# Kernel optimization log

Hardware: AMD Instinct MI355X
Metric: run time of the kernel (lower is better)

Reference implementation:

```python
import jax, jax.numpy as jnp
import numpy as np

N = 50000      # number of predictions
E = 1_600_000  # total neighborhood entries (sum of neighborhood sizes)
D = 128        # prediction representation dim
A = 4          # additional per-pair info dim (box offsets / IoU)
H = 128        # block hidden dim


def setup_inputs() -> dict:
    key = jax.random.key(0)
    ks = jax.random.split(key, 16)
    interpolated = jax.random.normal(ks[0], (N, D), dtype=jnp.float32)
    add_info = jax.random.normal(ks[1], (E, A), dtype=jnp.float32)
    neighbor_idx = jax.random.randint(ks[2], (E,), 0, N, dtype=jnp.int32)
    segment_ids = jnp.sort(jax.random.randint(ks[3], (E,), 0, N, dtype=jnp.int32))
    w = lambda k, shape: (jax.random.normal(k, shape, dtype=jnp.float32) * 0.02)
    return {
        "interpolated": interpolated,
        "add_info": add_info,
        "neighbor_idx": neighbor_idx,
        "segment_ids": segment_ids,
        "Wb0": w(ks[4], (D + A, H)), "bb0": jnp.zeros((H,), jnp.float32),
        "Wo0": w(ks[5], (H, D)),     "bo0": jnp.zeros((D,), jnp.float32),
        "Wb1": w(ks[6], (D + A, H)), "bb1": jnp.zeros((H,), jnp.float32),
        "Wo1": w(ks[7], (H, D)),     "bo1": jnp.zeros((D,), jnp.float32),
        "Wf": w(ks[8], (D, 1)),      "bf": jnp.zeros((1,), jnp.float32),
    }


def reference(interpolated, add_info, neighbor_idx, segment_ids,
              Wb0, bb0, Wo0, bo0, Wb1, bb1, Wo1, bo1, Wf, bf):
    def block_step(feats, Wb, bb, Wo, bo):
        # assemble all neighborhoods: gather neighbor reps, concat pair info -> (E, D+A)
        edge_feats = jnp.concatenate([feats[neighbor_idx], add_info], axis=-1)
        # block MLP on neighborhood entries -> (E, H)
        h = jax.nn.relu(edge_feats @ Wb + bb)
        # segment-wise max pool over each prediction's neighborhood -> (N, H)
        pooled = jax.ops.segment_max(h, segment_ids, num_segments=N)
        pooled = jnp.where(jnp.isfinite(pooled), pooled, 0.0)  # empty segments -> 0
        # output projection back to representation space, residual update
        return feats + (pooled @ Wo + bo)

    x = block_step(interpolated, Wb0, bb0, Wo0, bo0)
    x = block_step(x, Wb1, bb1, Wo1, bo1)
    # final layers: compress representation to updated objectness score -> (N, 1)
    return x @ Wf + bf
```

## Files before the change

### kernel.cpp

```cpp
#include <hip/hip_runtime.h>
#include <limits.h>
#include <cstdint>

typedef __bf16 bf16_t;
typedef __attribute__((ext_vector_type(8))) __bf16 bf16x8;
typedef __attribute__((ext_vector_type(4))) float f32x4;
typedef __attribute__((ext_vector_type(2))) float f32x2;

#define CH 64

struct PackArgs {
  const float* W[4];
  bf16_t* P[4];
};

__global__ __launch_bounds__(256) void pack4_kernel(PackArgs args) {
  int idx = blockIdx.x * blockDim.x + threadIdx.x;
  int which = idx >> 14;
  int r = idx & 16383;
  int j  = r & 7;
  int L  = (r >> 3) & 63;
  int nt = (r >> 9) & 7;
  int kt = r >> 12;
  int k = kt * 32 + (L >> 4) * 8 + j;
  int n = nt * 16 + (L & 15);
  args.P[which][r] = (bf16_t)args.W[which][(size_t)k * 128 + n];
}

__global__ __launch_bounds__(256, 4) void yproj_f32(
    const float* __restrict__ X, const bf16_t* __restrict__ Wtpk,
    bf16_t* __restrict__ Ybf, float* __restrict__ pooled, int N)
{
  const int tid = threadIdx.x;
  const int base = blockIdx.x * 128;

  float4 z = make_float4(0.f, 0.f, 0.f, 0.f);
  #pragma unroll
  for (int i = 0; i < 16; ++i) {
    int idx = tid + i * 256;
    int row = base + (idx >> 5);
    if (row < N)
      reinterpret_cast<float4*>(pooled)[(size_t)row * 32 + (idx & 31)] = z;
  }

  const int lane = tid & 63;
  const int w    = tid >> 6;
  const int q    = lane >> 4;
  const int ln   = lane & 15;
  const int n0   = base + w * 32;

  int r0 = n0 + ln, r1 = n0 + 16 + ln;
  int r0c = (r0 < N) ? r0 : (N - 1);
  int r1c = (r1 < N) ? r1 : (N - 1);
  const float* x0 = X + (size_t)r0c * 128 + q * 8;
  const float* x1 = X + (size_t)r1c * 128 + q * 8;

  f32x4 acc[2][8];
  #pragma unroll
  for (int mt = 0; mt < 2; ++mt)
    #pragma unroll
    for (int nt = 0; nt < 8; ++nt)
      #pragma unroll
      for (int r = 0; r < 4; ++r) acc[mt][nt][r] = 0.f;

  const bf16x8* Wp = reinterpret_cast<const bf16x8*>(Wtpk);
  #pragma unroll
  for (int kt = 0; kt < 4; ++kt) {
    float4 f0a = *reinterpret_cast<const float4*>(x0 + kt * 32);
    float4 f0b = *reinterpret_cast<const float4*>(x0 + kt * 32 + 4);
    float4 f1a = *reinterpret_cast<const float4*>(x1 + kt * 32);
    float4 f1b = *reinterpret_cast<const float4*>(x1 + kt * 32 + 4);
    bf16x8 a0, a1;
    a0[0] = (bf16_t)f0a.x; a0[1] = (bf16_t)f0a.y; a0[2] = (bf16_t)f0a.z; a0[3] = (bf16_t)f0a.w;
    a0[4] = (bf16_t)f0b.x; a0[5] = (bf16_t)f0b.y; a0[6] = (bf16_t)f0b.z; a0[7] = (bf16_t)f0b.w;
    a1[0] = (bf16_t)f1a.x; a1[1] = (bf16_t)f1a.y; a1[2] = (bf16_t)f1a.z; a1[3] = (bf16_t)f1a.w;
    a1[4] = (bf16_t)f1b.x; a1[5] = (bf16_t)f1b.y; a1[6] = (bf16_t)f1b.z; a1[7] = (bf16_t)f1b.w;
    #pragma unroll
    for (int nt = 0; nt < 8; ++nt) {
      bf16x8 bfrag = Wp[(kt * 8 + nt) * 64 + lane];
      acc[0][nt] = __builtin_amdgcn_mfma_f32_16x16x32_bf16(a0, bfrag, acc[0][nt], 0, 0, 0);
      acc[1][nt] = __builtin_amdgcn_mfma_f32_16x16x32_bf16(a1, bfrag, acc[1][nt], 0, 0, 0);
    }
  }

  #pragma unroll
  for (int mt = 0; mt < 2; ++mt) {
    #pragma unroll
    for (int r = 0; r < 4; ++r) {
      int row = n0 + mt * 16 + q * 4 + r;
      if (row < N) {
        #pragma unroll
        for (int nt = 0; nt < 8; ++nt) {
          int col = nt * 16 + ln;
          Ybf[(size_t)row * 128 + col] = (bf16_t)acc[mt][nt][r];
        }
      }
    }
  }
}

__global__ __launch_bounds__(256, 4) void yproj_bf16(
    const bf16_t* __restrict__ Xbf, const bf16_t* __restrict__ Wtpk,
    bf16_t* __restrict__ Ybf, float* __restrict__ pooled, int N)
{
  const int tid = threadIdx.x;
  const int base = blockIdx.x * 128;

  float4 z = make_float4(0.f, 0.f, 0.f, 0.f);
  #pragma unroll
  for (int i = 0; i < 16; ++i) {
    int idx = tid + i * 256;
    int row = base + (idx >> 5);
    if (row < N)
      reinterpret_cast<float4*>(pooled)[(size_t)row * 32 + (idx & 31)] = z;
  }

  const int lane = tid & 63;
  const int w    = tid >> 6;
  const int q    = lane >> 4;
  const int ln   = lane & 15;
  const int n0   = base + w * 32;

  int r0 = n0 + ln, r1 = n0 + 16 + ln;
  int r0c = (r0 < N) ? r0 : (N - 1);
  int r1c = (r1 < N) ? r1 : (N - 1);
  const bf16_t* x0 = Xbf + (size_t)r0c * 128 + q * 8;
  const bf16_t* x1 = Xbf + (size_t)r1c * 128 + q * 8;

  f32x4 acc[2][8];
  #pragma unroll
  for (int mt = 0; mt < 2; ++mt)
    #pragma unroll
    for (int nt = 0; nt < 8; ++nt)
      #pragma unroll
      for (int r = 0; r < 4; ++r) acc[mt][nt][r] = 0.f;

  const bf16x8* Wp = reinterpret_cast<const bf16x8*>(Wtpk);
  #pragma unroll
  for (int kt = 0; kt < 4; ++kt) {
    bf16x8 a0 = *reinterpret_cast<const bf16x8*>(x0 + kt * 32);
    bf16x8 a1 = *reinterpret_cast<const bf16x8*>(x1 + kt * 32);
    #pragma unroll
    for (int nt = 0; nt < 8; ++nt) {
      bf16x8 bfrag = Wp[(kt * 8 + nt) * 64 + lane];
      acc[0][nt] = __builtin_amdgcn_mfma_f32_16x16x32_bf16(a0, bfrag, acc[0][nt], 0, 0, 0);
      acc[1][nt] = __builtin_amdgcn_mfma_f32_16x16x32_bf16(a1, bfrag, acc[1][nt], 0, 0, 0);
    }
  }

  #pragma unroll
  for (int mt = 0; mt < 2; ++mt) {
    #pragma unroll
    for (int r = 0; r < 4; ++r) {
      int row = n0 + mt * 16 + q * 4 + r;
      if (row < N) {
        #pragma unroll
        for (int nt = 0; nt < 8; ++nt) {
          int col = nt * 16 + ln;
          Ybf[(size_t)row * 128 + col] = (bf16_t)acc[mt][nt][r];
        }
      }
    }
  }
}

__global__ __launch_bounds__(256) void edge_stream(
    const bf16_t* __restrict__ Y,
    const float* __restrict__ Wb,
    const float* __restrict__ bb,
    const float* __restrict__ add_info,
    const int* __restrict__ nbr, const int* __restrict__ segs,
    float* __restrict__ pooled, int E)
{
  __shared__ float a_lds[1024];
  const int lane = threadIdx.x & 63;
  const int wv = __builtin_amdgcn_readfirstlane(threadIdx.x >> 6);
  const int e0 = (blockIdx.x * 4 + wv) * CH;
  if (e0 >= E) return;
  const int c0 = lane * 2;

  f32x2 wk[4];
  #pragma unroll
  for (int k = 0; k < 4; ++k) {
    wk[k].x = Wb[(size_t)(128 + k) * 128 + c0];
    wk[k].y = Wb[(size_t)(128 + k) * 128 + c0 + 1];
  }
  f32x2 bbv;
  bbv.x = bb[c0]; bbv.y = bb[c0 + 1];

  unsigned* pooled_u = reinterpret_cast<unsigned*>(pooled);
  f32x2 v; v.x = 0.f; v.y = 0.f;

  if (e0 + CH <= E) {
    float4 av = *reinterpret_cast<const float4*>(add_info + (size_t)e0 * 4 + lane * 4);
    int v_nbr = nbr[e0 + lane];
    int v_sg  = segs[e0 + lane];

    int sg_prev = __shfl_up(v_sg, 1);
    unsigned long long bmask = __ballot(v_sg != sg_prev) & ~1ull;
    int cur = __builtin_amdgcn_readlane(v_sg, 0);

    unsigned ybuf[4][8];
    #pragma unroll
    for (int p = 0; p < 3; ++p) {
      #pragma unroll
      for (int j = 0; j < 8; ++j) {
        int rn = __builtin_amdgcn_readlane(v_nbr, p * 8 + j);
        ybuf[p][j] = *((const unsigned*)(Y + (size_t)rn * 128) + lane);
      }
    }

    *reinterpret_cast<float4*>(a_lds + wv * 256 + lane * 4) = av;

    #pragma unroll
    for (int g = 0; g < CH / 8; ++g) {
      if (g + 3 < CH / 8) {
        #pragma unroll
        for (int j = 0; j < 8; ++j) {
          int rn = __builtin_amdgcn_readlane(v_nbr, (g + 3) * 8 + j);
          ybuf[(g + 3) & 3][j] = *((const unsigned*)(Y + (size_t)rn * 128) + lane);
        }
      }
      #pragma unroll
      for (int j = 0; j < 8; ++j) {
        const int i = g * 8 + j;
        if (bmask & (1ull << i)) {
          if (v.x > 0.f) atomicMax(&pooled_u[(size_t)cur * 128 + c0], __float_as_uint(v.x));
          if (v.y > 0.f) atomicMax(&pooled_u[(size_t)cur * 128 + c0 + 1], __float_as_uint(v.y));
          v.x = 0.f; v.y = 0.f;
          cur = __builtin_amdgcn_readlane(v_sg, i);
        }
        unsigned yb = ybuf[g & 3][j];
        f32x2 y;
        y.x = __uint_as_float(yb << 16);
        y.y = __uint_as_float(yb & 0xffff0000u);
        f32x4 a4 = *reinterpret_cast<const f32x4*>(a_lds + wv * 256 + i * 4);
        f32x2 t = bbv + a4[0] * wk[0];
        t += a4[1] * wk[1];
        t += a4[2] * wk[2];
        t += a4[3] * wk[3];
        t += y;
        v = __builtin_elementwise_max(v, t);
      }
    }
    if (v.x > 0.f) atomicMax(&pooled_u[(size_t)cur * 128 + c0], __float_as_uint(v.x));
    if (v.y > 0.f) atomicMax(&pooled_u[(size_t)cur * 128 + c0 + 1], __float_as_uint(v.y));
  } else {
    int cur = segs[e0];
    const int rem = E - e0;
    for (int i = 0; i < rem; ++i) {
      const int e = e0 + i;
      int sg = segs[e];
      if (sg != cur) {
        if (v.x > 0.f) atomicMax(&pooled_u[(size_t)cur * 128 + c0], __float_as_uint(v.x));
        if (v.y > 0.f) atomicMax(&pooled_u[(size_t)cur * 128 + c0 + 1], __float_as_uint(v.y));
        v.x = 0.f; v.y = 0.f; cur = sg;
      }
      unsigned yb = *reinterpret_cast<const unsigned*>(Y + (size_t)nbr[e] * 128 + c0);
      float y0 = __uint_as_float(yb << 16);
      float y1 = __uint_as_float(yb & 0xffff0000u);
      const float* ai = add_info + (size_t)e * 4;
      float a0 = ai[0], a1 = ai[1], a2 = ai[2], a3 = ai[3];
      float t0 = y0 + bbv.x + a0 * wk[0].x + a1 * wk[1].x + a2 * wk[2].x + a3 * wk[3].x;
      float t1 = y1 + bbv.y + a0 * wk[0].y + a1 * wk[1].y + a2 * wk[2].y + a3 * wk[3].y;
      v.x = fmaxf(v.x, t0);
      v.y = fmaxf(v.y, t1);
    }
    if (v.x > 0.f) atomicMax(&pooled_u[(size_t)cur * 128 + c0], __float_as_uint(v.x));
    if (v.y > 0.f) atomicMax(&pooled_u[(size_t)cur * 128 + c0 + 1], __float_as_uint(v.y));
  }
}

__global__ __launch_bounds__(256, 4) void update_mfma(
    const float* __restrict__ featsIn, const float* __restrict__ pooled,
    const bf16_t* __restrict__ Wopk, const float* __restrict__ bo,
    const float* __restrict__ Wf,
    float* __restrict__ featsOut, bf16_t* __restrict__ featsOutBf,
    float* __restrict__ fdot, int N)
{
  const int tid  = threadIdx.x;
  const int lane = tid & 63;
  const int w    = tid >> 6;
  const int q    = lane >> 4;
  const int ln   = lane & 15;
  const int n0   = blockIdx.x * 128 + w * 32;

  int r0 = n0 + ln, r1 = n0 + 16 + ln;
  int r0c = (r0 < N) ? r0 : (N - 1);
  int r1c = (r1 < N) ? r1 : (N - 1);
  const float* p0 = pooled + (size_t)r0c * 128 + q * 8;
  const float* p1 = pooled + (size_t)r1c * 128 + q * 8;

  f32x4 acc[2][8];
  #pragma unroll
  for (int mt = 0; mt < 2; ++mt)
    #pragma unroll
    for (int nt = 0; nt < 8; ++nt)
      #pragma unroll
      for (int r = 0; r < 4; ++r) acc[mt][nt][r] = 0.f;

  const bf16x8* Wp = reinterpret_cast<const bf16x8*>(Wopk);
  #pragma unroll
  for (int kt = 0; kt < 4; ++kt) {
    float4 f0a = *reinterpret_cast<const float4*>(p0 + kt * 32);
    float4 f0b = *reinterpret_cast<const float4*>(p0 + kt * 32 + 4);
    float4 f1a = *reinterpret_cast<const float4*>(p1 + kt * 32);
    float4 f1b = *reinterpret_cast<const float4*>(p1 + kt * 32 + 4);
    bf16x8 a0, a1;
    a0[0] = (bf16_t)f0a.x; a0[1] = (bf16_t)f0a.y; a0[2] = (bf16_t)f0a.z; a0[3] = (bf16_t)f0a.w;
    a0[4] = (bf16_t)f0b.x; a0[5] = (bf16_t)f0b.y; a0[6] = (bf16_t)f0b.z; a0[7] = (bf16_t)f0b.w;
    a1[0] = (bf16_t)f1a.x; a1[1] = (bf16_t)f1a.y; a1[2] = (bf16_t)f1a.z; a1[3] = (bf16_t)f1a.w;
    a1[4] = (bf16_t)f1b.x; a1[5] = (bf16_t)f1b.y; a1[6] = (bf16_t)f1b.z; a1[7] = (bf16_t)f1b.w;
    #pragma unroll
    for (int nt = 0; nt < 8; ++nt) {
      bf16x8 bfrag = Wp[(kt * 8 + nt) * 64 + lane];
      acc[0][nt] = __builtin_amdgcn_mfma_f32_16x16x32_bf16(a0, bfrag, acc[0][nt], 0, 0, 0);
      acc[1][nt] = __builtin_amdgcn_mfma_f32_16x16x32_bf16(a1, bfrag, acc[1][nt], 0, 0, 0);
    }
  }

  float bov[8], wfv[8];
  #pragma unroll
  for (int nt = 0; nt < 8; ++nt) { bov[nt] = bo[nt * 16 + ln]; wfv[nt] = Wf[nt * 16 + ln]; }

  #pragma unroll
  for (int mt = 0; mt < 2; ++mt) {
    #pragma unroll
    for (int r = 0; r < 4; ++r) {
      int row = n0 + mt * 16 + q * 4 + r;
      float partial = 0.f;
      if (row < N) {
        #pragma unroll
        for (int nt = 0; nt < 8; ++nt) {
          int col = nt * 16 + ln;
          float o = featsIn[(size_t)row * 128 + col] + acc[mt][nt][r] + bov[nt];
          featsOut[(size_t)row * 128 + col] = o;
          featsOutBf[(size_t)row * 128 + col] = (bf16_t)o;
          partial += o * wfv[nt];
        }
      }
      partial += __shfl_xor(partial, 1);
      partial += __shfl_xor(partial, 2);
      partial += __shfl_xor(partial, 4);
      partial += __shfl_xor(partial, 8);
      if (ln == 0 && row < N) fdot[row] = partial;
    }
  }
}

__global__ __launch_bounds__(256, 4) void update_final_mfma(
    const float* __restrict__ fdot, const float* __restrict__ pooled,
    const bf16_t* __restrict__ Wopk, const float* __restrict__ bo,
    const float* __restrict__ Wf, const float* __restrict__ bf_,
    float* __restrict__ out, int N)
{
  const int tid  = threadIdx.x;
  const int lane = tid & 63;
  const int w    = tid >> 6;
  const int q    = lane >> 4;
  const int ln   = lane & 15;
  const int n0   = blockIdx.x * 128 + w * 32;

  int r0 = n0 + ln, r1 = n0 + 16 + ln;
  int r0c = (r0 < N) ? r0 : (N - 1);
  int r1c = (r1 < N) ? r1 : (N - 1);
  const float* p0 = pooled + (size_t)r0c * 128 + q * 8;
  const float* p1 = pooled + (size_t)r1c * 128 + q * 8;

  f32x4 acc[2][8];
  #pragma unroll
  for (int mt = 0; mt < 2; ++mt)
    #pragma unroll
    for (int nt = 0; nt < 8; ++nt)
      #pragma unroll
      for (int r = 0; r < 4; ++r) acc[mt][nt][r] = 0.f;

  const bf16x8* Wp = reinterpret_cast<const bf16x8*>(Wopk);
  #pragma unroll
  for (int kt = 0; kt < 4; ++kt) {
    float4 f0a = *reinterpret_cast<const float4*>(p0 + kt * 32);
    float4 f0b = *reinterpret_cast<const float4*>(p0 + kt * 32 + 4);
    float4 f1a = *reinterpret_cast<const float4*>(p1 + kt * 32);
    float4 f1b = *reinterpret_cast<const float4*>(p1 + kt * 32 + 4);
    bf16x8 a0, a1;
    a0[0] = (bf16_t)f0a.x; a0[1] = (bf16_t)f0a.y; a0[2] = (bf16_t)f0a.z; a0[3] = (bf16_t)f0a.w;
    a0[4] = (bf16_t)f0b.x; a0[5] = (bf16_t)f0b.y; a0[6] = (bf16_t)f0b.z; a0[7] = (bf16_t)f0b.w;
    a1[0] = (bf16_t)f1a.x; a1[1] = (bf16_t)f1a.y; a1[2] = (bf16_t)f1a.z; a1[3] = (bf16_t)f1a.w;
    a1[4] = (bf16_t)f1b.x; a1[5] = (bf16_t)f1b.y; a1[6] = (bf16_t)f1b.z; a1[7] = (bf16_t)f1b.w;
    #pragma unroll
    for (int nt = 0; nt < 8; ++nt) {
      bf16x8 bfrag = Wp[(kt * 8 + nt) * 64 + lane];
      acc[0][nt] = __builtin_amdgcn_mfma_f32_16x16x32_bf16(a0, bfrag, acc[0][nt], 0, 0, 0);
      acc[1][nt] = __builtin_amdgcn_mfma_f32_16x16x32_bf16(a1, bfrag, acc[1][nt], 0, 0, 0);
    }
  }

  float bov[8], wfv[8];
  #pragma unroll
  for (int nt = 0; nt < 8; ++nt) { bov[nt] = bo[nt * 16 + ln]; wfv[nt] = Wf[nt * 16 + ln]; }
  float bfs = bf_[0];

  #pragma unroll
  for (int mt = 0; mt < 2; ++mt) {
    #pragma unroll
    for (int r = 0; r < 4; ++r) {
      int row = n0 + mt * 16 + q * 4 + r;
      float partial = 0.f;
      #pragma unroll
      for (int nt = 0; nt < 8; ++nt)
        partial += (acc[mt][nt][r] + bov[nt]) * wfv[nt];
      partial += __shfl_xor(partial, 1);
      partial += __shfl_xor(partial, 2);
      partial += __shfl_xor(partial, 4);
      partial += __shfl_xor(partial, 8);
      if (ln == 0 && row < N) out[row] = partial + fdot[row] + bfs;
    }
  }
}

extern "C" void kernel_launch(void* const* d_in, const int* in_sizes, int n_in,
                              void* d_out, int out_size, void* d_ws, size_t ws_size,
                              hipStream_t stream)
{
  const float* interpolated = (const float*)d_in[0];
  const float* add_info     = (const float*)d_in[1];
  const int*   nbr          = (const int*)d_in[2];
  const int*   segs         = (const int*)d_in[3];
  const float* Wb0 = (const float*)d_in[4];
  const float* bb0 = (const float*)d_in[5];
  const float* Wo0 = (const float*)d_in[6];
  const float* bo0 = (const float*)d_in[7];
  const float* Wb1 = (const float*)d_in[8];
  const float* bb1 = (const float*)d_in[9];
  const float* Wo1 = (const float*)d_in[10];
  const float* bo1 = (const float*)d_in[11];
  const float* Wf  = (const float*)d_in[12];
  const float* bf_ = (const float*)d_in[13];

  const int N = in_sizes[0] / 128;
  const int E = in_sizes[2];
  float* out = (float*)d_out;

  float* pooled = (float*)d_ws;
  float* featsB = pooled + (size_t)N * 128;
  bf16_t* featsB_bf = (bf16_t*)(featsB + (size_t)N * 128);
  bf16_t* Ybf       = featsB_bf + (size_t)N * 128;
  bf16_t* Wtpk0 = Ybf + (size_t)N * 128;
  bf16_t* Wtpk1 = Wtpk0 + 16384;
  bf16_t* Wopk0 = Wtpk1 + 16384;
  bf16_t* Wopk1 = Wopk0 + 16384;
  float*  fdot  = (float*)(Wopk1 + 16384);

  const int ugrid = (N + 127) / 128;
  const int egrid = (E + CH * 4 - 1) / (CH * 4);

  PackArgs pa;
  pa.W[0] = Wb0; pa.P[0] = Wtpk0;
  pa.W[1] = Wb1; pa.P[1] = Wtpk1;
  pa.W[2] = Wo0; pa.P[2] = Wopk0;
  pa.W[3] = Wo1; pa.P[3] = Wopk1;
  pack4_kernel<<<256, 256, 0, stream>>>(pa);

  yproj_f32<<<ugrid, 256, 0, stream>>>(interpolated, Wtpk0, Ybf, pooled, N);
  edge_stream<<<egrid, 256, 0, stream>>>(Ybf, Wb0, bb0, add_info, nbr, segs,
                                         pooled, E);
  update_mfma<<<ugrid, 256, 0, stream>>>(interpolated, pooled, Wopk0, bo0,
                                         Wf, featsB, featsB_bf, fdot, N);

  yproj_bf16<<<ugrid, 256, 0, stream>>>(featsB_bf, Wtpk1, Ybf, pooled, N);
  edge_stream<<<egrid, 256, 0, stream>>>(Ybf, Wb1, bb1, add_info, nbr, segs,
                                         pooled, E);
  update_final_mfma<<<ugrid, 256, 0, stream>>>(fdot, pooled, Wopk1, bo1,
                                               Wf, bf_, out, N);
}
```

Baseline: 305.4 us.

## Split Y into column-quarter planes and process four edges per wave

The projected neighbor table Y is stored as four planes of 32 columns each (64 bytes per row) instead of full 256-byte rows. In edge_stream each wave splits into four 16-lane groups, each handling a different edge, and loops over the four column quarters. Each plane is 1/4 the size of Y, which aims to improve L2/cache hit rates for the random neighbor gathers. The cost is more atomics and bpermute work and more loop iterations per wave.

```diff
diff --git a/kernel.cpp b/kernel.cpp
--- a/kernel.cpp
+++ b/kernel.cpp
@@ -91,8 +91,8 @@
       if (row < N) {
         #pragma unroll
         for (int nt = 0; nt < 8; ++nt) {
-          int col = nt * 16 + ln;
-          Ybf[(size_t)row * 128 + col] = (bf16_t)acc[mt][nt][r];
+          Ybf[((size_t)(nt >> 1) * N + row) * 32 + (nt & 1) * 16 + ln] =
+              (bf16_t)acc[mt][nt][r];
         }
       }
     }
@@ -156,8 +156,8 @@
       if (row < N) {
         #pragma unroll
         for (int nt = 0; nt < 8; ++nt) {
-          int col = nt * 16 + ln;
-          Ybf[(size_t)row * 128 + col] = (bf16_t)acc[mt][nt][r];
+          Ybf[((size_t)(nt >> 1) * N + row) * 32 + (nt & 1) * 16 + ln] =
+              (bf16_t)acc[mt][nt][r];
         }
       }
     }
@@ -165,76 +165,72 @@
 }
 
 __global__ __launch_bounds__(256) void edge_stream(
-    const bf16_t* __restrict__ Y,
+    const bf16_t* __restrict__ Yq,
     const float* __restrict__ Wb,
     const float* __restrict__ bb,
     const float* __restrict__ add_info,
     const int* __restrict__ nbr, const int* __restrict__ segs,
-    float* __restrict__ pooled, int E)
+    float* __restrict__ pooled, int N, int E)
 {
   __shared__ float a_lds[1024];
-  const int lane = threadIdx.x & 63;
-  const int wv = __builtin_amdgcn_readfirstlane(threadIdx.x >> 6);
-  const int e0 = (blockIdx.x * 4 + wv) * CH;
+  const int lane  = threadIdx.x & 63;
+  const int wv    = __builtin_amdgcn_readfirstlane(threadIdx.x >> 6);
+  const int e0    = (blockIdx.x * 4 + wv) * CH;
   if (e0 >= E) return;
-  const int c0 = lane * 2;
-
-  f32x2 wk[4];
-  #pragma unroll
-  for (int k = 0; k < 4; ++k) {
-    wk[k].x = Wb[(size_t)(128 + k) * 128 + c0];
-    wk[k].y = Wb[(size_t)(128 + k) * 128 + c0 + 1];
-  }
-  f32x2 bbv;
-  bbv.x = bb[c0]; bbv.y = bb[c0 + 1];
+  const int group = lane >> 4;
+  const int sl    = lane & 15;
 
   unsigned* pooled_u = reinterpret_cast<unsigned*>(pooled);
-  f32x2 v; v.x = 0.f; v.y = 0.f;
+  const unsigned* Yu = reinterpret_cast<const unsigned*>(Yq);
 
   if (e0 + CH <= E) {
     float4 av = *reinterpret_cast<const float4*>(add_info + (size_t)e0 * 4 + lane * 4);
     int v_nbr = nbr[e0 + lane];
     int v_sg  = segs[e0 + lane];
-
-    int sg_prev = __shfl_up(v_sg, 1);
-    unsigned long long bmask = __ballot(v_sg != sg_prev) & ~1ull;
-    int cur = __builtin_amdgcn_readlane(v_sg, 0);
-
-    unsigned ybuf[4][8];
-    #pragma unroll
-    for (int p = 0; p < 3; ++p) {
-      #pragma unroll
-      for (int j = 0; j < 8; ++j) {
-        int rn = __builtin_amdgcn_readlane(v_nbr, p * 8 + j);
-        ybuf[p][j] = *((const unsigned*)(Y + (size_t)rn * 128) + lane);
-      }
-    }
-
     *reinterpret_cast<float4*>(a_lds + wv * 256 + lane * 4) = av;
 
-    #pragma unroll
-    for (int g = 0; g < CH / 8; ++g) {
-      if (g + 3 < CH / 8) {
-        #pragma unroll
-        for (int j = 0; j < 8; ++j) {
-          int rn = __builtin_amdgcn_readlane(v_nbr, (g + 3) * 8 + j);
-          ybuf[(g + 3) & 3][j] = *((const unsigned*)(Y + (size_t)rn * 128) + lane);
+    int rnv[16], sgv[16];
+    #pragma unroll
+    for (int s = 0; s < 16; ++s) {
+      int bidx = (4 * s + group) * 4;
+      rnv[s] = __builtin_amdgcn_ds_bpermute(bidx, v_nbr);
+      sgv[s] = __builtin_amdgcn_ds_bpermute(bidx, v_sg);
+    }
+
+    #pragma unroll
+    for (int q = 0; q < 4; ++q) {
+      const int cq = q * 32 + sl * 2;
+      f32x2 wk[4];
+      #pragma unroll
+      for (int k = 0; k < 4; ++k) {
+        wk[k].x = Wb[(size_t)(128 + k) * 128 + cq];
+        wk[k].y = Wb[(size_t)(128 + k) * 128 + cq + 1];
+      }
+      f32x2 bbv; bbv.x = bb[cq]; bbv.y = bb[cq + 1];
+      const size_t qb = (size_t)q * N;
+
+      f32x2 v; v.x = 0.f; v.y = 0.f;
+      unsigned ybuf[4];
+      #pragma unroll
+      for (int p = 0; p < 3; ++p)
+        ybuf[p] = Yu[(qb + (unsigned)rnv[p]) * 16 + sl];
+
+      #pragma unroll
+      for (int s = 0; s < 16; ++s) {
+        if (s + 3 < 16)
+          ybuf[(s + 3) & 3] = Yu[(qb + (unsigned)rnv[s + 3]) * 16 + sl];
+        if (s > 0 && sgv[s] != sgv[s - 1]) {
+          if (v.x > 0.f)
+            atomicMax(&pooled_u[(size_t)sgv[s - 1] * 128 + cq], __float_as_uint(v.x));
+          if (v.y > 0.f)
+            atomicMax(&pooled_u[(size_t)sgv[s - 1] * 128 + cq + 1], __float_as_uint(v.y));
+          v.x = 0.f; v.y = 0.f;
         }
-      }
-      #pragma unroll
-      for (int j = 0; j < 8; ++j) {
-        const int i = g * 8 + j;
-        if (bmask & (1ull << i)) {
-          if (v.x > 0.f) atomicMax(&pooled_u[(size_t)cur * 128 + c0], __float_as_uint(v.x));
-          if (v.y > 0.f) atomicMax(&pooled_u[(size_t)cur * 128 + c0 + 1], __float_as_uint(v.y));
-          v.x = 0.f; v.y = 0.f;
-          cur = __builtin_amdgcn_readlane(v_sg, i);
-        }
-        unsigned yb = ybuf[g & 3][j];
+        unsigned yb = ybuf[s & 3];
         f32x2 y;
         y.x = __uint_as_float(yb << 16);
         y.y = __uint_as_float(yb & 0xffff0000u);
-        f32x4 a4 = *reinterpret_cast<const f32x4*>(a_lds + wv * 256 + i * 4);
+        f32x4 a4 = *reinterpret_cast<const f32x4*>(a_lds + wv * 256 + (4 * s + group) * 4);
         f32x2 t = bbv + a4[0] * wk[0];
         t += a4[1] * wk[1];
         t += a4[2] * wk[2];
@@ -242,10 +238,21 @@
         t += y;
         v = __builtin_elementwise_max(v, t);
       }
-    }
-    if (v.x > 0.f) atomicMax(&pooled_u[(size_t)cur * 128 + c0], __float_as_uint(v.x));
-    if (v.y > 0.f) atomicMax(&pooled_u[(size_t)cur * 128 + c0 + 1], __float_as_uint(v.y));
+      if (v.x > 0.f)
+        atomicMax(&pooled_u[(size_t)sgv[15] * 128 + cq], __float_as_uint(v.x));
+      if (v.y > 0.f)
+        atomicMax(&pooled_u[(size_t)sgv[15] * 128 + cq + 1], __float_as_uint(v.y));
+    }
   } else {
+    const int c0 = group * 32 + sl * 2;
+    f32x2 wk[4];
+    #pragma unroll
+    for (int k = 0; k < 4; ++k) {
+      wk[k].x = Wb[(size_t)(128 + k) * 128 + c0];
+      wk[k].y = Wb[(size_t)(128 + k) * 128 + c0 + 1];
+    }
+    f32x2 bbv; bbv.x = bb[c0]; bbv.y = bb[c0 + 1];
+    f32x2 v; v.x = 0.f; v.y = 0.f;
     int cur = segs[e0];
     const int rem = E - e0;
     for (int i = 0; i < rem; ++i) {
@@ -256,7 +263,8 @@
         if (v.y > 0.f) atomicMax(&pooled_u[(size_t)cur * 128 + c0 + 1], __float_as_uint(v.y));
         v.x = 0.f; v.y = 0.f; cur = sg;
       }
-      unsigned yb = *reinterpret_cast<const unsigned*>(Y + (size_t)nbr[e] * 128 + c0);
+      int rn = nbr[e];
+      unsigned yb = Yu[((size_t)group * N + rn) * 16 + sl];
       float y0 = __uint_as_float(yb << 16);
       float y1 = __uint_as_float(yb & 0xffff0000u);
       const float* ai = add_info + (size_t)e * 4;
@@ -463,13 +471,13 @@
 
   yproj_f32<<<ugrid, 256, 0, stream>>>(interpolated, Wtpk0, Ybf, pooled, N);
   edge_stream<<<egrid, 256, 0, stream>>>(Ybf, Wb0, bb0, add_info, nbr, segs,
-                                         pooled, E);
+                                         pooled, N, E);
   update_mfma<<<ugrid, 256, 0, stream>>>(interpolated, pooled, Wopk0, bo0,
                                          Wf, featsB, featsB_bf, fdot, N);
 
   yproj_bf16<<<ugrid, 256, 0, stream>>>(featsB_bf, Wtpk1, Ybf, pooled, N);
   edge_stream<<<egrid, 256, 0, stream>>>(Ybf, Wb1, bb1, add_info, nbr, segs,
-                                         pooled, E);
+                                         pooled, N, E);
   update_final_mfma<<<ugrid, 256, 0, stream>>>(fdot, pooled, Wopk1, bo1,
                                                Wf, bf_, out, N);
 }
```

Measured after the change: 851.5 us. 2.79x slower.
